# Performance work log

Measured on AMD Instinct MI355X. Metric: run time of the kernel, lower is better.

Reference implementation:

```python
import jax, jax.numpy as jnp
import numpy as np

NEG_SLOPE = 0.2  # PyG GATConv default leaky_relu slope


def gat_layer(x, src, dst, W, a_src, a_dst, bias, heads, out_ch, concat):
    """One GATConv layer (PyG semantics, shared lin for src/dst).
    x: [N, F_in]; src/dst: [E] int; W: [F_in, heads*out_ch];
    a_src/a_dst: [heads, out_ch]; bias: [heads*out_ch] or [out_ch]."""
    N = x.shape[0]
    h = (x @ W).reshape(N, heads, out_ch)              # [N, H, C]
    al_s = jnp.sum(h * a_src, axis=-1)                 # [N, H]
    al_d = jnp.sum(h * a_dst, axis=-1)                 # [N, H]
    e = jax.nn.leaky_relu(al_s[src] + al_d[dst], NEG_SLOPE)  # [E, H]
    # segment softmax over incoming edges of each destination node
    m = jax.ops.segment_max(e, dst, num_segments=N)
    m = jnp.where(jnp.isfinite(m), m, 0.0)             # nodes w/o edges
    ex = jnp.exp(e - m[dst])
    denom = jax.ops.segment_sum(ex, dst, num_segments=N)
    alpha = ex / denom[dst]                            # [E, H]; denom>0 via self-loops
    out = jax.ops.segment_sum(alpha[:, :, None] * h[src], dst, num_segments=N)  # [N,H,C]
    out = out.reshape(N, heads * out_ch) if concat else out.mean(axis=1)
    return out + bias


def setup_inputs() -> dict:
    key = jax.random.key(0)
    ks = jax.random.split(key, 10)
    N, E, F_in, Ch = 50000, 800000, 5, 64
    glorot = lambda k, shp: jax.random.uniform(
        k, shp, jnp.float32, -1.0, 1.0) * np.sqrt(6.0 / (shp[0] + shp[-1]))
    return {
        "x": jax.random.normal(ks[0], (N, F_in), jnp.float32),
        "edge_index": jax.random.randint(ks[1], (2, E), 0, N, jnp.int32),
        "W1": glorot(ks[2], (F_in, 4 * Ch)),
        "a_src1": glorot(ks[3], (4, Ch)),
        "a_dst1": glorot(ks[4], (4, Ch)),
        "b1": jnp.zeros((4 * Ch,), jnp.float32),
        "W2": glorot(ks[5], (4 * Ch, Ch)),
        "a_src2": glorot(ks[6], (1, Ch)),
        "a_dst2": glorot(ks[7], (1, Ch)),
        "b2": jnp.zeros((Ch,), jnp.float32),
    }


def reference(x, edge_index, W1, a_src1, a_dst1, b1, W2, a_src2, a_dst2, b2):
    N = x.shape[0]
    loops = jnp.arange(N, dtype=edge_index.dtype)      # PyG adds self-loops by default
    src = jnp.concatenate([edge_index[0], loops])
    dst = jnp.concatenate([edge_index[1], loops])
    h = gat_layer(x, src, dst, W1, a_src1, a_dst1, b1, heads=4, out_ch=64, concat=True)
    h = jax.nn.relu(h)
    h = gat_layer(h, src, dst, W2, a_src2, a_dst2, b2, heads=1, out_ch=64, concat=False)
    return h.mean(axis=0)                              # [64]
```

## Files before the change

### kernel.cpp

```cpp
#include <hip/hip_runtime.h>
#include <hip/hip_bf16.h>

#define NEG_SLOPE 0.2f

typedef __attribute__((ext_vector_type(8))) short short8;
typedef __attribute__((ext_vector_type(4))) float f32x4;

__device__ __forceinline__ float wave_sum64(float v) {
#pragma unroll
    for (int off = 32; off >= 1; off >>= 1) v += __shfl_xor(v, off, 64);
    return v;
}

__device__ __forceinline__ float bf2f(unsigned short u) {
    return __uint_as_float((unsigned int)u << 16);
}

__device__ __forceinline__ unsigned short f2bf(float f) {
    __hip_bfloat16 hb = __float2bfloat16(f);
    return *reinterpret_cast<unsigned short*>(&hb);
}

__global__ __launch_bounds__(256) void kb1_deg(
    const int* __restrict__ ei, int E, int Etot, int* __restrict__ deg) {
    int e = blockIdx.x * 256 + threadIdx.x;
    if (e >= Etot) return;
    int dst = (e < E) ? ei[E + e] : e - E;
    atomicAdd(&deg[dst], 1);
}

__global__ __launch_bounds__(256) void kb2_alloc(
    const int* __restrict__ deg, int N, int* __restrict__ counter,
    int* __restrict__ row_ptr, int* __restrict__ row_end,
    int* __restrict__ row_cur) {
    int n = blockIdx.x * 256 + threadIdx.x;
    int lane = threadIdx.x & 63;
    int d = (n < N) ? deg[n] : 0;
    int x = d;
#pragma unroll
    for (int off = 1; off < 64; off <<= 1) {
        int y = __shfl_up(x, off, 64);
        if (lane >= off) x += y;
    }
    int total = __shfl(x, 63, 64);
    int base = 0;
    if (lane == 63) base = atomicAdd(counter, total);
    base = __shfl(base, 63, 64);
    if (n < N) {
        int beg = base + x - d;
        row_ptr[n] = beg; row_cur[n] = beg; row_end[n] = beg + d;
    }
}

__global__ __launch_bounds__(256) void kb3_scatter(
    const int* __restrict__ ei, int E, int Etot,
    int* __restrict__ row_cur, int* __restrict__ csr_src) {
    int e = blockIdx.x * 256 + threadIdx.x;
    if (e >= Etot) return;
    int src, dst;
    if (e < E) { src = ei[e]; dst = ei[E + e]; }
    else       { src = dst = e - E; }
    int pos = atomicAdd(&row_cur[dst], 1);
    csr_src[pos] = src;
}

__global__ __launch_bounds__(256) void kw_pack(
    const float* __restrict__ W2, unsigned short* __restrict__ W2t) {
    int i = blockIdx.x * 256 + threadIdx.x;
    if (i >= 64 * 256) return;
    int c = i >> 8, k = i & 255;
    W2t[c * 256 + k] = f2bf(W2[k * 64 + c]);
}

__global__ __launch_bounds__(256) void k1_node1(
    const float* __restrict__ x, const float* __restrict__ W1,
    const float* __restrict__ a_src1, const float* __restrict__ a_dst1,
    unsigned short* __restrict__ h1b, float* __restrict__ al_s1,
    float* __restrict__ al_d1, int N) {
    int n = blockIdx.x;
    if (n >= N) return;
    int t = threadIdx.x;
    float h = 0.f;
#pragma unroll
    for (int k = 0; k < 5; ++k) h = fmaf(x[n * 5 + k], W1[k * 256 + t], h);
    int head = t >> 6, ch = t & 63;
    h1b[(size_t)n * 256 + ch * 4 + head] = f2bf(h);
    float s = wave_sum64(h * a_src1[t]);
    float d = wave_sum64(h * a_dst1[t]);
    if (ch == 0) {
        al_s1[n * 4 + head] = s;
        al_d1[n * 4 + head] = d;
    }
}

__global__ __launch_bounds__(256) void k2_gather1(
    const int* __restrict__ csr_src, const int* __restrict__ row_ptr,
    const int* __restrict__ row_end,
    const unsigned short* __restrict__ h1b, const float* __restrict__ al_s1,
    const float* __restrict__ al_d1, const float* __restrict__ b1,
    unsigned short* __restrict__ x2b, int N) {
    int wave = threadIdx.x >> 6, lane = threadIdx.x & 63;
    int n = blockIdx.x * 4 + wave;
    if (n >= N) return;
    int beg = row_ptr[n], end = row_end[n];
    const float4 ad = *reinterpret_cast<const float4*>(&al_d1[n * 4]);
    float a0 = 0.f, a1 = 0.f, a2 = 0.f, a3 = 0.f;
    float d0 = 0.f, d1 = 0.f, d2 = 0.f, d3 = 0.f;
    for (int base = beg; base < end; base += 64) {
        int nn = min(64, end - base);
        int srcv = (base + lane < end) ? csr_src[base + lane] : 0;
        for (int i = 0; i < nn; ++i) {
            int src = __shfl(srcv, i, 64);
            const float4 as = *reinterpret_cast<const float4*>(&al_s1[src * 4]);
            float v0 = as.x + ad.x, v1 = as.y + ad.y, v2 = as.z + ad.z, v3 = as.w + ad.w;
            v0 = v0 > 0.f ? v0 : NEG_SLOPE * v0;
            v1 = v1 > 0.f ? v1 : NEG_SLOPE * v1;
            v2 = v2 > 0.f ? v2 : NEG_SLOPE * v2;
            v3 = v3 > 0.f ? v3 : NEG_SLOPE * v3;
            float ex0 = __expf(v0), ex1 = __expf(v1), ex2 = __expf(v2), ex3 = __expf(v3);
            const ushort4 u = *reinterpret_cast<const ushort4*>(
                &h1b[(size_t)src * 256 + lane * 4]);
            a0 = fmaf(ex0, bf2f(u.x), a0); d0 += ex0;
            a1 = fmaf(ex1, bf2f(u.y), a1); d1 += ex1;
            a2 = fmaf(ex2, bf2f(u.z), a2); d2 += ex2;
            a3 = fmaf(ex3, bf2f(u.w), a3); d3 += ex3;
        }
    }
    unsigned short* xo = &x2b[(size_t)n * 256];
    float r;
    r = a0 / d0 + b1[0 * 64 + lane]; xo[0 * 64 + lane] = f2bf(r > 0.f ? r : 0.f);
    r = a1 / d1 + b1[1 * 64 + lane]; xo[1 * 64 + lane] = f2bf(r > 0.f ? r : 0.f);
    r = a2 / d2 + b1[2 * 64 + lane]; xo[2 * 64 + lane] = f2bf(r > 0.f ? r : 0.f);
    r = a3 / d3 + b1[3 * 64 + lane]; xo[3 * 64 + lane] = f2bf(r > 0.f ? r : 0.f);
}

__global__ __launch_bounds__(256) void k3_mfma(
    const unsigned short* __restrict__ x2b, const unsigned short* __restrict__ W2t,
    const float* __restrict__ a_src2, const float* __restrict__ a_dst2,
    float* __restrict__ h2, float* __restrict__ al_s2, float* __restrict__ al_d2,
    int N) {
    int w = threadIdx.x >> 6, l = threadIdx.x & 63;
    int m0 = blockIdx.x * 64 + w * 16;
    if (m0 >= N) return;
    int lr = l & 15, lg = l >> 4;

    short8 b0[8], b1f[8], b2f[8], b3f[8];
#pragma unroll
    for (int kk = 0; kk < 8; ++kk) {
        b0[kk]  = *reinterpret_cast<const short8*>(&W2t[(0 * 16 + lr) * 256 + kk * 32 + lg * 8]);
        b1f[kk] = *reinterpret_cast<const short8*>(&W2t[(1 * 16 + lr) * 256 + kk * 32 + lg * 8]);
        b2f[kk] = *reinterpret_cast<const short8*>(&W2t[(2 * 16 + lr) * 256 + kk * 32 + lg * 8]);
        b3f[kk] = *reinterpret_cast<const short8*>(&W2t[(3 * 16 + lr) * 256 + kk * 32 + lg * 8]);
    }
    short8 a[8];
#pragma unroll
    for (int kk = 0; kk < 8; ++kk)
        a[kk] = *reinterpret_cast<const short8*>(&x2b[(size_t)(m0 + lr) * 256 + kk * 32 + lg * 8]);

    f32x4 acc0 = {0.f, 0.f, 0.f, 0.f}, acc1 = acc0, acc2 = acc0, acc3 = acc0;
#pragma unroll
    for (int kk = 0; kk < 8; ++kk) {
        acc0 = __builtin_amdgcn_mfma_f32_16x16x32_bf16(a[kk], b0[kk],  acc0, 0, 0, 0);
        acc1 = __builtin_amdgcn_mfma_f32_16x16x32_bf16(a[kk], b1f[kk], acc1, 0, 0, 0);
        acc2 = __builtin_amdgcn_mfma_f32_16x16x32_bf16(a[kk], b2f[kk], acc2, 0, 0, 0);
        acc3 = __builtin_amdgcn_mfma_f32_16x16x32_bf16(a[kk], b3f[kk], acc3, 0, 0, 0);
    }

#pragma unroll
    for (int j = 0; j < 4; ++j) {
        float* hr = &h2[(size_t)(m0 + lg * 4 + j) * 64];
        hr[0 * 16 + lr] = acc0[j];
        hr[1 * 16 + lr] = acc1[j];
        hr[2 * 16 + lr] = acc2[j];
        hr[3 * 16 + lr] = acc3[j];
    }

    float sA0 = a_src2[0 * 16 + lr], sA1 = a_src2[1 * 16 + lr];
    float sA2 = a_src2[2 * 16 + lr], sA3 = a_src2[3 * 16 + lr];
    float sD0 = a_dst2[0 * 16 + lr], sD1 = a_dst2[1 * 16 + lr];
    float sD2 = a_dst2[2 * 16 + lr], sD3 = a_dst2[3 * 16 + lr];
    float p0 = acc0[0] * sA0 + acc1[0] * sA1 + acc2[0] * sA2 + acc3[0] * sA3;
    float p1 = acc0[1] * sA0 + acc1[1] * sA1 + acc2[1] * sA2 + acc3[1] * sA3;
    float p2 = acc0[2] * sA0 + acc1[2] * sA1 + acc2[2] * sA2 + acc3[2] * sA3;
    float p3 = acc0[3] * sA0 + acc1[3] * sA1 + acc2[3] * sA2 + acc3[3] * sA3;
    float q0 = acc0[0] * sD0 + acc1[0] * sD1 + acc2[0] * sD2 + acc3[0] * sD3;
    float q1 = acc0[1] * sD0 + acc1[1] * sD1 + acc2[1] * sD2 + acc3[1] * sD3;
    float q2 = acc0[2] * sD0 + acc1[2] * sD1 + acc2[2] * sD2 + acc3[2] * sD3;
    float q3 = acc0[3] * sD0 + acc1[3] * sD1 + acc2[3] * sD2 + acc3[3] * sD3;
#pragma unroll
    for (int off = 1; off <= 8; off <<= 1) {
        p0 += __shfl_xor(p0, off, 64); p1 += __shfl_xor(p1, off, 64);
        p2 += __shfl_xor(p2, off, 64); p3 += __shfl_xor(p3, off, 64);
        q0 += __shfl_xor(q0, off, 64); q1 += __shfl_xor(q1, off, 64);
        q2 += __shfl_xor(q2, off, 64); q3 += __shfl_xor(q3, off, 64);
    }
    if (lr == 0) {
        int r0 = m0 + lg * 4;
        al_s2[r0 + 0] = p0; al_s2[r0 + 1] = p1; al_s2[r0 + 2] = p2; al_s2[r0 + 3] = p3;
        al_d2[r0 + 0] = q0; al_d2[r0 + 1] = q1; al_d2[r0 + 2] = q2; al_d2[r0 + 3] = q3;
    }
}

__global__ __launch_bounds__(256) void k4_gather2(
    const int* __restrict__ csr_src, const int* __restrict__ row_ptr,
    const int* __restrict__ row_end,
    const float* __restrict__ h2, const float* __restrict__ al_s2,
    const float* __restrict__ al_d2, float* __restrict__ o2, int N) {
    int wave = threadIdx.x >> 6, lane = threadIdx.x & 63;
    int n = blockIdx.x * 4 + wave;
    if (n >= N) return;
    int beg = row_ptr[n], end = row_end[n];
    float ad = al_d2[n];
    float a = 0.f, d = 0.f;
    for (int base = beg; base < end; base += 64) {
        int nn = min(64, end - base);
        bool ok = (base + lane < end);
        int srcv = ok ? csr_src[base + lane] : 0;
        float asv = ok ? al_s2[srcv] : 0.f;
        for (int i = 0; i < nn; ++i) {
            int src = __shfl(srcv, i, 64);
            float as = __shfl(asv, i, 64);
            float v = as + ad;
            v = v > 0.f ? v : NEG_SLOPE * v;
            float ex = __expf(v);
            a = fmaf(ex, h2[(size_t)src * 64 + lane], a);
            d += ex;
        }
    }
    o2[(size_t)n * 64 + lane] = a / d;
}

__global__ __launch_bounds__(64) void k5_final(
    const float* __restrict__ o2, const float* __restrict__ b2,
    float* __restrict__ out, int N) {
    int lane = threadIdx.x;
    float acc = 0.f;
    for (int n = blockIdx.x; n < N; n += gridDim.x)
        acc += o2[(size_t)n * 64 + lane];
    float v = acc * (1.f / (float)N);
    if (blockIdx.x == 0) v += b2[lane];
    atomicAdd(&out[lane], v);
}

extern "C" void kernel_launch(void* const* d_in, const int* in_sizes, int n_in,
                              void* d_out, int out_size, void* d_ws, size_t ws_size,
                              hipStream_t stream) {
    const float* x   = (const float*)d_in[0];
    const int*   ei  = (const int*)d_in[1];
    const float* W1  = (const float*)d_in[2];
    const float* as1 = (const float*)d_in[3];
    const float* ad1 = (const float*)d_in[4];
    const float* b1  = (const float*)d_in[5];
    const float* W2  = (const float*)d_in[6];
    const float* as2 = (const float*)d_in[7];
    const float* ad2 = (const float*)d_in[8];
    const float* b2  = (const float*)d_in[9];
    float* out = (float*)d_out;

    const int F_in = in_sizes[2] / 256;
    const int N = in_sizes[0] / F_in;
    const int E = in_sizes[1] / 2;
    const int Etot = E + N;

    unsigned short* h1b = (unsigned short*)d_ws;
    unsigned short* x2b = h1b + (size_t)N * 256;
    float* h2    = (float*)(x2b + (size_t)N * 256);
    float* al_s1 = h2 + (size_t)N * 64;
    float* al_d1 = al_s1 + (size_t)N * 4;
    unsigned short* W2t = (unsigned short*)(al_d1 + (size_t)N * 4);
    int* deg     = (int*)(W2t + 64 * 256);
    int* row_cur = deg + N;
    int* row_ptr = row_cur + N;
    int* row_end = row_ptr + N;
    int* counter = row_end + N;
    int* csr_src = counter + 1;
    float* o2    = (float*)h1b;
    float* al_s2 = al_s1;
    float* al_d2 = al_d1;

    hipMemsetAsync(deg, 0, (size_t)N * sizeof(int), stream);
    hipMemsetAsync(counter, 0, sizeof(int), stream);
    hipMemsetAsync(out, 0, 64 * sizeof(float), stream);

    kb1_deg    <<<(Etot + 255) / 256, 256, 0, stream>>>(ei, E, Etot, deg);
    kb2_alloc  <<<(N + 255) / 256, 256, 0, stream>>>(deg, N, counter, row_ptr, row_end, row_cur);
    kb3_scatter<<<(Etot + 255) / 256, 256, 0, stream>>>(ei, E, Etot, row_cur, csr_src);
    kw_pack    <<<64, 256, 0, stream>>>(W2, W2t);

    k1_node1  <<<N, 256, 0, stream>>>(x, W1, as1, ad1, h1b, al_s1, al_d1, N);
    k2_gather1<<<(N + 3) / 4, 256, 0, stream>>>(csr_src, row_ptr, row_end, h1b, al_s1, al_d1, b1, x2b, N);
    k3_mfma   <<<(N + 63) / 64, 256, 0, stream>>>(x2b, W2t, as2, ad2, h2, al_s2, al_d2, N);
    k4_gather2<<<(N + 3) / 4, 256, 0, stream>>>(csr_src, row_ptr, row_end, h2, al_s2, al_d2, o2, N);
    k5_final  <<<256, 64, 0, stream>>>(o2, b2, out, N);
}
```

Measured before the change: 426.4 us.

## Split edge softmax weight computation from feature gather in both GAT layers

Each gather kernel is split in two. The first kernel computes the per-edge exp weights lane-parallel, writes them to a workspace buffer, and reduces the per-node denominators with a wave reduction. The second kernel then gathers features using the precomputed weights. This removes the redundant serial exp and attention-logit loads that every lane used to repeat inside the inner edge loop. In exchange it adds two kernel launches, an extra write and read of an edge-sized weight buffer, and a larger workspace.

```diff
diff --git a/kernel.cpp b/kernel.cpp
--- a/kernel.cpp
+++ b/kernel.cpp
@@ -93,45 +93,72 @@
     }
 }
 
-__global__ __launch_bounds__(256) void k2_gather1(
+__global__ __launch_bounds__(256) void k2a_wts(
     const int* __restrict__ csr_src, const int* __restrict__ row_ptr,
-    const int* __restrict__ row_end,
-    const unsigned short* __restrict__ h1b, const float* __restrict__ al_s1,
-    const float* __restrict__ al_d1, const float* __restrict__ b1,
-    unsigned short* __restrict__ x2b, int N) {
+    const int* __restrict__ row_end, const float* __restrict__ al_s1,
+    const float* __restrict__ al_d1, float* __restrict__ ew,
+    float* __restrict__ denom1, int N) {
     int wave = threadIdx.x >> 6, lane = threadIdx.x & 63;
     int n = blockIdx.x * 4 + wave;
     if (n >= N) return;
     int beg = row_ptr[n], end = row_end[n];
     const float4 ad = *reinterpret_cast<const float4*>(&al_d1[n * 4]);
-    float a0 = 0.f, a1 = 0.f, a2 = 0.f, a3 = 0.f;
     float d0 = 0.f, d1 = 0.f, d2 = 0.f, d3 = 0.f;
     for (int base = beg; base < end; base += 64) {
-        int nn = min(64, end - base);
-        int srcv = (base + lane < end) ? csr_src[base + lane] : 0;
-        for (int i = 0; i < nn; ++i) {
-            int src = __shfl(srcv, i, 64);
+        int e = base + lane;
+        if (e < end) {
+            int src = csr_src[e];
             const float4 as = *reinterpret_cast<const float4*>(&al_s1[src * 4]);
             float v0 = as.x + ad.x, v1 = as.y + ad.y, v2 = as.z + ad.z, v3 = as.w + ad.w;
             v0 = v0 > 0.f ? v0 : NEG_SLOPE * v0;
             v1 = v1 > 0.f ? v1 : NEG_SLOPE * v1;
             v2 = v2 > 0.f ? v2 : NEG_SLOPE * v2;
             v3 = v3 > 0.f ? v3 : NEG_SLOPE * v3;
-            float ex0 = __expf(v0), ex1 = __expf(v1), ex2 = __expf(v2), ex3 = __expf(v3);
+            float4 ex;
+            ex.x = __expf(v0); ex.y = __expf(v1); ex.z = __expf(v2); ex.w = __expf(v3);
+            *reinterpret_cast<float4*>(&ew[(size_t)e * 4]) = ex;
+            d0 += ex.x; d1 += ex.y; d2 += ex.z; d3 += ex.w;
+        }
+    }
+    d0 = wave_sum64(d0); d1 = wave_sum64(d1);
+    d2 = wave_sum64(d2); d3 = wave_sum64(d3);
+    if (lane == 0) {
+        float4 dn = {d0, d1, d2, d3};
+        *reinterpret_cast<float4*>(&denom1[n * 4]) = dn;
+    }
+}
+
+__global__ __launch_bounds__(256) void k2b_gather1(
+    const int* __restrict__ csr_src, const int* __restrict__ row_ptr,
+    const int* __restrict__ row_end, const unsigned short* __restrict__ h1b,
+    const float* __restrict__ ew, const float* __restrict__ denom1,
+    const float* __restrict__ b1, unsigned short* __restrict__ x2b, int N) {
+    int wave = threadIdx.x >> 6, lane = threadIdx.x & 63;
+    int n = blockIdx.x * 4 + wave;
+    if (n >= N) return;
+    int beg = row_ptr[n], end = row_end[n];
+    float a0 = 0.f, a1 = 0.f, a2 = 0.f, a3 = 0.f;
+    for (int base = beg; base < end; base += 64) {
+        int nn = min(64, end - base);
+        int srcv = (base + lane < end) ? csr_src[base + lane] : 0;
+        for (int i = 0; i < nn; ++i) {
+            int src = __shfl(srcv, i, 64);
+            const float4 w = *reinterpret_cast<const float4*>(&ew[(size_t)(base + i) * 4]);
             const ushort4 u = *reinterpret_cast<const ushort4*>(
                 &h1b[(size_t)src * 256 + lane * 4]);
-            a0 = fmaf(ex0, bf2f(u.x), a0); d0 += ex0;
-            a1 = fmaf(ex1, bf2f(u.y), a1); d1 += ex1;
-            a2 = fmaf(ex2, bf2f(u.z), a2); d2 += ex2;
-            a3 = fmaf(ex3, bf2f(u.w), a3); d3 += ex3;
+            a0 = fmaf(w.x, bf2f(u.x), a0);
+            a1 = fmaf(w.y, bf2f(u.y), a1);
+            a2 = fmaf(w.z, bf2f(u.z), a2);
+            a3 = fmaf(w.w, bf2f(u.w), a3);
         }
     }
+    const float4 dn = *reinterpret_cast<const float4*>(&denom1[n * 4]);
     unsigned short* xo = &x2b[(size_t)n * 256];
     float r;
-    r = a0 / d0 + b1[0 * 64 + lane]; xo[0 * 64 + lane] = f2bf(r > 0.f ? r : 0.f);
-    r = a1 / d1 + b1[1 * 64 + lane]; xo[1 * 64 + lane] = f2bf(r > 0.f ? r : 0.f);
-    r = a2 / d2 + b1[2 * 64 + lane]; xo[2 * 64 + lane] = f2bf(r > 0.f ? r : 0.f);
-    r = a3 / d3 + b1[3 * 64 + lane]; xo[3 * 64 + lane] = f2bf(r > 0.f ? r : 0.f);
+    r = a0 / dn.x + b1[0 * 64 + lane]; xo[0 * 64 + lane] = f2bf(r > 0.f ? r : 0.f);
+    r = a1 / dn.y + b1[1 * 64 + lane]; xo[1 * 64 + lane] = f2bf(r > 0.f ? r : 0.f);
+    r = a2 / dn.z + b1[2 * 64 + lane]; xo[2 * 64 + lane] = f2bf(r > 0.f ? r : 0.f);
+    r = a3 / dn.w + b1[3 * 64 + lane]; xo[3 * 64 + lane] = f2bf(r > 0.f ? r : 0.f);
 }
 
 __global__ __launch_bounds__(256) void k3_mfma(
@@ -201,33 +228,52 @@
     }
 }
 
-__global__ __launch_bounds__(256) void k4_gather2(
+__global__ __launch_bounds__(256) void k4a_wts(
     const int* __restrict__ csr_src, const int* __restrict__ row_ptr,
-    const int* __restrict__ row_end,
-    const float* __restrict__ h2, const float* __restrict__ al_s2,
-    const float* __restrict__ al_d2, float* __restrict__ o2, int N) {
+    const int* __restrict__ row_end, const float* __restrict__ al_s2,
+    const float* __restrict__ al_d2, float* __restrict__ ew2,
+    float* __restrict__ denom2, int N) {
     int wave = threadIdx.x >> 6, lane = threadIdx.x & 63;
     int n = blockIdx.x * 4 + wave;
     if (n >= N) return;
     int beg = row_ptr[n], end = row_end[n];
     float ad = al_d2[n];
-    float a = 0.f, d = 0.f;
+    float dsum = 0.f;
+    for (int base = beg; base < end; base += 64) {
+        int e = base + lane;
+        if (e < end) {
+            int src = csr_src[e];
+            float v = al_s2[src] + ad;
+            v = v > 0.f ? v : NEG_SLOPE * v;
+            float ex = __expf(v);
+            ew2[e] = ex;
+            dsum += ex;
+        }
+    }
+    dsum = wave_sum64(dsum);
+    if (lane == 0) denom2[n] = dsum;
+}
+
+__global__ __launch_bounds__(256) void k4b_gather2(
+    const int* __restrict__ csr_src, const int* __restrict__ row_ptr,
+    const int* __restrict__ row_end, const float* __restrict__ h2,
+    const float* __restrict__ ew2, const float* __restrict__ denom2,
+    float* __restrict__ o2, int N) {
+    int wave = threadIdx.x >> 6, lane = threadIdx.x & 63;
+    int n = blockIdx.x * 4 + wave;
+    if (n >= N) return;
+    int beg = row_ptr[n], end = row_end[n];
+    float a = 0.f;
     for (int base = beg; base < end; base += 64) {
         int nn = min(64, end - base);
-        bool ok = (base + lane < end);
-        int srcv = ok ? csr_src[base + lane] : 0;
-        float asv = ok ? al_s2[srcv] : 0.f;
+        int srcv = (base + lane < end) ? csr_src[base + lane] : 0;
         for (int i = 0; i < nn; ++i) {
             int src = __shfl(srcv, i, 64);
-            float as = __shfl(asv, i, 64);
-            float v = as + ad;
-            v = v > 0.f ? v : NEG_SLOPE * v;
-            float ex = __expf(v);
-            a = fmaf(ex, h2[(size_t)src * 64 + lane], a);
-            d += ex;
+            float w = ew2[base + i];
+            a = fmaf(w, h2[(size_t)src * 64 + lane], a);
         }
     }
-    o2[(size_t)n * 64 + lane] = a / d;
+    o2[(size_t)n * 64 + lane] = a / denom2[n];
 }
 
 __global__ __launch_bounds__(64) void k5_final(
@@ -267,7 +313,9 @@
     float* h2    = (float*)(x2b + (size_t)N * 256);
     float* al_s1 = h2 + (size_t)N * 64;
     float* al_d1 = al_s1 + (size_t)N * 4;
-    unsigned short* W2t = (unsigned short*)(al_d1 + (size_t)N * 4);
+    float* ew    = al_d1 + (size_t)N * 4;
+    float* denom1= ew + (size_t)Etot * 4;
+    unsigned short* W2t = (unsigned short*)(denom1 + (size_t)N * 4);
     int* deg     = (int*)(W2t + 64 * 256);
     int* row_cur = deg + N;
     int* row_ptr = row_cur + N;
@@ -277,6 +325,8 @@
     float* o2    = (float*)h1b;
     float* al_s2 = al_s1;
     float* al_d2 = al_d1;
+    float* ew2   = ew;
+    float* denom2= denom1;
 
     hipMemsetAsync(deg, 0, (size_t)N * sizeof(int), stream);
     hipMemsetAsync(counter, 0, sizeof(int), stream);
@@ -287,9 +337,11 @@
     kb3_scatter<<<(Etot + 255) / 256, 256, 0, stream>>>(ei, E, Etot, row_cur, csr_src);
     kw_pack    <<<64, 256, 0, stream>>>(W2, W2t);
 
-    k1_node1  <<<N, 256, 0, stream>>>(x, W1, as1, ad1, h1b, al_s1, al_d1, N);
-    k2_gather1<<<(N + 3) / 4, 256, 0, stream>>>(csr_src, row_ptr, row_end, h1b, al_s1, al_d1, b1, x2b, N);
-    k3_mfma   <<<(N + 63) / 64, 256, 0, stream>>>(x2b, W2t, as2, ad2, h2, al_s2, al_d2, N);
-    k4_gather2<<<(N + 3) / 4, 256, 0, stream>>>(csr_src, row_ptr, row_end, h2, al_s2, al_d2, o2, N);
-    k5_final  <<<256, 64, 0, stream>>>(o2, b2, out, N);
-}
+    k1_node1   <<<N, 256, 0, stream>>>(x, W1, as1, ad1, h1b, al_s1, al_d1, N);
+    k2a_wts    <<<(N + 3) / 4, 256, 0, stream>>>(csr_src, row_ptr, row_end, al_s1, al_d1, ew, denom1, N);
+    k2b_gather1<<<(N + 3) / 4, 256, 0, stream>>>(csr_src, row_ptr, row_end, h1b, ew, denom1, b1, x2b, N);
+    k3_mfma    <<<(N + 63) / 64, 256, 0, stream>>>(x2b, W2t, as2, ad2, h2, al_s2, al_d2, N);
+    k4a_wts    <<<(N + 3) / 4, 256, 0, stream>>>(csr_src, row_ptr, row_end, al_s2, al_d2, ew2, denom2, N);
+    k4b_gather2<<<(N + 3) / 4, 256, 0, stream>>>(csr_src, row_ptr, row_end, h2, ew2, denom2, o2, N);
+    k5_final   <<<256, 64, 0, stream>>>(o2, b2, out, N);
+}
```

Result: slower. 442.5 us (+3.8%).
